# Kernel optimization log

Hardware: AMD Instinct MI355X
Metric: run time of the kernel (lower is better)

## Reference

```python
import jax, jax.numpy as jnp
import numpy as np

N_HEADS = 32
N_KV_HEADS = 8
HEAD_DIM = 64
DIM = 2048
MAX_CTX = 2048
N_REP = N_HEADS // N_KV_HEADS


def setup_inputs() -> dict:
    key = jax.random.key(0)
    ks = jax.random.split(key, 8)
    B, S = 1, 2048
    x = jax.random.normal(ks[0], (B, S, DIM), dtype=jnp.float32)
    # RoPE frequencies (real cos/sin, [S, head_dim//2])
    inv_freq = 1.0 / (10000.0 ** (np.arange(0, HEAD_DIM, 2, dtype=np.float32) / HEAD_DIM))
    t = np.arange(S, dtype=np.float32)
    freqs = np.outer(t, inv_freq)  # [S, HEAD_DIM//2]
    freqs_cos = jnp.asarray(np.cos(freqs), dtype=jnp.float32)
    freqs_sin = jnp.asarray(np.sin(freqs), dtype=jnp.float32)
    input_pos = jnp.arange(S, dtype=jnp.int32)
    scale = 0.02
    wq = jax.random.normal(ks[1], (N_HEADS * HEAD_DIM, DIM), dtype=jnp.float32) * scale
    wk = jax.random.normal(ks[2], (N_KV_HEADS * HEAD_DIM, DIM), dtype=jnp.float32) * scale
    wv = jax.random.normal(ks[3], (N_KV_HEADS * HEAD_DIM, DIM), dtype=jnp.float32) * scale
    wo = jax.random.normal(ks[4], (DIM, N_HEADS * HEAD_DIM), dtype=jnp.float32) * scale
    k_cache = jnp.zeros((B, N_KV_HEADS, MAX_CTX, HEAD_DIM), dtype=jnp.float32)
    v_cache = jnp.zeros((B, N_KV_HEADS, MAX_CTX, HEAD_DIM), dtype=jnp.float32)
    return {"x": x, "freqs_cos": freqs_cos, "freqs_sin": freqs_sin,
            "input_pos": input_pos, "wq": wq, "wk": wk, "wv": wv, "wo": wo,
            "k_cache": k_cache, "v_cache": v_cache}


def _apply_rope(x, cos, sin):
    # x: [B, S, H, HEAD_DIM]; cos/sin: [S, HEAD_DIM//2]
    xr = x[..., 0::2]
    xi = x[..., 1::2]
    c = cos[None, :, None, :]
    s = sin[None, :, None, :]
    out_r = xr * c - xi * s
    out_i = xr * s + xi * c
    # interleave back: stack on new trailing axis then flatten pairs
    out = jnp.stack([out_r, out_i], axis=-1)
    return out.reshape(x.shape)


def reference(x, freqs_cos, freqs_sin, input_pos, wq, wk, wv, wo, k_cache, v_cache):
    B, S, _ = x.shape
    q = (x @ wq.T).reshape(B, S, N_HEADS, HEAD_DIM)
    k = (x @ wk.T).reshape(B, S, N_KV_HEADS, HEAD_DIM)
    v = (x @ wv.T).reshape(B, S, N_KV_HEADS, HEAD_DIM)
    q = _apply_rope(q, freqs_cos, freqs_sin)
    k = _apply_rope(k, freqs_cos, freqs_sin)
    q = q.transpose(0, 2, 1, 3)   # [B, H, S, D]
    k = k.transpose(0, 2, 1, 3)   # [B, KV, S, D]
    v = v.transpose(0, 2, 1, 3)
    # KV-cache scatter update at input_pos
    k_full = k_cache.at[:, :, input_pos].set(k)   # [B, KV, MAX_CTX, D]
    v_full = v_cache.at[:, :, input_pos].set(v)
    # causal mask rows gathered at input_pos: [S, MAX_CTX]
    causal = jnp.tril(jnp.ones((MAX_CTX, MAX_CTX), dtype=bool))
    attn_mask = causal[input_pos]
    # GQA repeat_interleave along head dim
    k_rep = jnp.repeat(k_full, N_REP, axis=1)    # [B, H, MAX_CTX, D]
    v_rep = jnp.repeat(v_full, N_REP, axis=1)
    scale = 1.0 / jnp.sqrt(jnp.asarray(HEAD_DIM, dtype=x.dtype))
    scores = jnp.einsum('bhsd,bhtd->bhst', q, k_rep) * scale  # [B, H, S, MAX_CTX]
    neg = jnp.asarray(jnp.finfo(scores.dtype).min, dtype=scores.dtype)
    scores = jnp.where(attn_mask[None, None, :, :], scores, neg)
    attn = jax.nn.softmax(scores, axis=-1)
    y = jnp.einsum('bhst,bhtd->bhsd', attn, v_rep)  # [B, H, S, D]
    y = y.transpose(0, 2, 1, 3).reshape(B, S, N_HEADS * HEAD_DIM)
    return y @ wo.T
```

## Files before the change

### kernel.cpp

```cpp
#include <hip/hip_runtime.h>


typedef __attribute__((ext_vector_type(8))) __bf16 bf16x8;
typedef __attribute__((ext_vector_type(4))) float f32x4;

#define S_LEN 2048
#define DIMN  2048
#define NH    32
#define NKV   8
#define HD    64
#define QKVF  3072

__device__ __forceinline__ ushort f2bf(float f) {
  union { float f; unsigned u; } v; v.f = f;
  unsigned r = v.u + 0x7fffu + ((v.u >> 16) & 1u);
  return (ushort)(r >> 16);
}
__device__ __forceinline__ unsigned pack_bf2_rz(float a, float b) {
  union { float f; unsigned u; } va, vb; va.f = a; vb.f = b;
  return (va.u >> 16) | (vb.u & 0xffff0000u);
}
__device__ __forceinline__ float bf2f(ushort u) {
  union { unsigned u; float f; } v; v.u = ((unsigned)u) << 16;
  return v.f;
}
__device__ __forceinline__ void gld_lds16(const void* g, void* l) {
  __builtin_amdgcn_global_load_lds(
      (const __attribute__((address_space(1))) unsigned int*)g,
      (__attribute__((address_space(3))) unsigned int*)l, 16, 0, 0);
}

__global__ __launch_bounds__(256) void convert_all(
    const float* __restrict__ x, const float* __restrict__ wq,
    const float* __restrict__ wk, const float* __restrict__ wv,
    const float* __restrict__ wo, ushort* __restrict__ xb,
    ushort* __restrict__ wqkvb, ushort* __restrict__ wob) {
  const size_t NX = 4u * 1024 * 1024;
  const size_t NK = 1024 * 1024;
  size_t idx = ((size_t)blockIdx.x * 256 + threadIdx.x) * 4;
  const float* src; ushort* dst;
  if (idx < NX)                { src = x  + idx;                  dst = xb + idx; }
  else if (idx < 2 * NX)       { src = wq + (idx - NX);           dst = wqkvb + (idx - NX); }
  else if (idx < 2 * NX + NK)  { src = wk + (idx - 2 * NX);       dst = wqkvb + NX + (idx - 2 * NX); }
  else if (idx < 2 * NX + 2*NK){ src = wv + (idx - 2 * NX - NK);  dst = wqkvb + NX + NK + (idx - 2 * NX - NK); }
  else                         { src = wo + (idx - 2 * NX - 2*NK);dst = wob + (idx - 2 * NX - 2 * NK); }
  float4 v = *(const float4*)src;
  ushort4 o; o.x = f2bf(v.x); o.y = f2bf(v.y); o.z = f2bf(v.z); o.w = f2bf(v.w);
  *(ushort4*)dst = o;
}

template <int OUT_BF16, int BM, int BN>
__global__ __launch_bounds__(256) void gemm_bt(
    const ushort* __restrict__ A, const ushort* __restrict__ B,
    void* __restrict__ Cv, int M, int N, int K) {
  constexpr int IB = BM / 32;
  constexpr int JB = BN / 32;
  constexpr int NGA = BM / 8;
  constexpr int GPW = (BM + BN) / 32;
  __shared__ __align__(16) ushort As[2][BM * 64];
  __shared__ __align__(16) ushort Bs[2][BN * 64];
  const int n0 = blockIdx.x * BN, m0 = blockIdx.y * BM;
  const int t = threadIdx.x;
  const int lane = t & 63, wave = t >> 6;
  const int wm = (wave >> 1) * (BM / 2), wn = (wave & 1) * (BN / 2);
  const int col = lane & 15, quad = lane >> 4;
  const int sw = col & 7;
  const int lrow = lane >> 3;
  const int scol = ((lane & 7) ^ lrow) * 8;
  f32x4 acc[IB][JB] = {};

  auto stage = [&](int b, int kk) {
#pragma unroll
    for (int c = 0; c < GPW; ++c) {
      int g = wave * GPW + c;
      if (g < NGA)
        gld_lds16(&A[(size_t)(m0 + g * 8 + lrow) * K + kk + scol], &As[b][g * 8 * 64]);
      else
        gld_lds16(&B[(size_t)(n0 + (g - NGA) * 8 + lrow) * K + kk + scol],
                  &Bs[b][(g - NGA) * 8 * 64]);
    }
  };

  stage(0, 0);
  __syncthreads();
  for (int kk = 0; kk < K; kk += 64) {
    const int b = (kk >> 6) & 1;
    if (kk + 64 < K) stage(b ^ 1, kk + 64);
#pragma unroll
    for (int c = 0; c < 2; ++c) {
      const int chs = ((c * 4 + quad) ^ sw) * 8;
      bf16x8 af[IB], bfr[JB];
#pragma unroll
      for (int i = 0; i < IB; ++i)
        af[i] = *(const bf16x8*)&As[b][(wm + i * 16 + col) * 64 + chs];
#pragma unroll
      for (int j = 0; j < JB; ++j)
        bfr[j] = *(const bf16x8*)&Bs[b][(wn + j * 16 + col) * 64 + chs];
#pragma unroll
      for (int i = 0; i < IB; ++i)
#pragma unroll
        for (int j = 0; j < JB; ++j)
          acc[i][j] = __builtin_amdgcn_mfma_f32_16x16x32_bf16(af[i], bfr[j], acc[i][j], 0, 0, 0);
    }
    __syncthreads();
  }
#pragma unroll
  for (int i = 0; i < IB; ++i)
#pragma unroll
    for (int r = 0; r < 4; ++r) {
      int m = m0 + wm + i * 16 + quad * 4 + r;
      if (OUT_BF16) {
        ushort* C = (ushort*)Cv;
#pragma unroll
        for (int j = 0; j < JB; ++j)
          C[(size_t)m * N + n0 + wn + j * 16 + col] = f2bf(acc[i][j][r]);
      } else {
        float* C = (float*)Cv;
#pragma unroll
        for (int j = 0; j < JB; ++j)
          C[(size_t)m * N + n0 + wn + j * 16 + col] = acc[i][j][r];
      }
    }
}

__global__ __launch_bounds__(256) void rope_layout(
    const ushort* __restrict__ qkv, const float* __restrict__ fc,
    const float* __restrict__ fs, ushort* __restrict__ qb,
    ushort* __restrict__ kb, ushort* __restrict__ vt) {
  __shared__ ushort T[64][72];
  const int hh = blockIdx.x;
  const int s0 = blockIdx.y * 256;
  const int t = threadIdx.x;
  if (hh < 32) {
    ushort* dst = qb + (size_t)hh * S_LEN * 64;
    const float qs = 0.18033688011112042f;
    const int sr = t >> 4, dc = (t & 15) * 4, i0 = (t & 15) * 2;
#pragma unroll 4
    for (int pass = 0; pass < 16; ++pass) {
      int s = s0 + pass * 16 + sr;
      ushort4 vv = *(const ushort4*)&qkv[(size_t)s * QKVF + hh * 64 + dc];
      float2 cc = *(const float2*)&fc[s * 32 + i0];
      float2 ss = *(const float2*)&fs[s * 32 + i0];
      float xr0 = bf2f(vv.x), xi0 = bf2f(vv.y), xr1 = bf2f(vv.z), xi1 = bf2f(vv.w);
      ushort4 ov;
      ov.x = f2bf((xr0 * cc.x - xi0 * ss.x) * qs); ov.y = f2bf((xr0 * ss.x + xi0 * cc.x) * qs);
      ov.z = f2bf((xr1 * cc.y - xi1 * ss.y) * qs); ov.w = f2bf((xr1 * ss.y + xi1 * cc.y) * qs);
      *(ushort4*)&dst[(size_t)s * 64 + dc] = ov;
    }
  } else if (hh < 40) {
    const int kh2 = hh - 32;
    const int sr8 = t >> 3;
    const int ch = t & 7;
#pragma unroll 2
    for (int pass = 0; pass < 8; ++pass) {
      int s = s0 + pass * 32 + sr8;
      ushort in[8], out[8];
      *(int4*)&in[0] = *(const int4*)&qkv[(size_t)s * QKVF + 2048 + kh2 * 64 + ch * 8];
      float4 cc = *(const float4*)&fc[s * 32 + ch * 4];
      float4 ss4 = *(const float4*)&fs[s * 32 + ch * 4];
      const float* cp = &cc.x; const float* sp = &ss4.x;
#pragma unroll
      for (int i = 0; i < 4; ++i) {
        float xr = bf2f(in[2 * i]), xi = bf2f(in[2 * i + 1]);
        out[2 * i]     = f2bf(xr * cp[i] - xi * sp[i]);
        out[2 * i + 1] = f2bf(xr * sp[i] + xi * cp[i]);
      }
      int r = s & 63, tile = s >> 6;
      size_t pos = ((size_t)(kh2 * 32 + tile)) * 4096 +
                   ((size_t)(((ch >> 2) * 4 + (r >> 4)) * 64 + (ch & 3) * 16 + (r & 15))) * 8;
      *(int4*)&kb[pos] = *(const int4*)&out[0];
    }
  } else {
    const int vh = hh - 40;
    for (int sub = 0; sub < 4; ++sub) {
      int sb = s0 + sub * 64;
      int sr = t >> 2, dc = (t & 3) * 16;
      ushort tmp[16];
      *(int4*)&tmp[0] = *(const int4*)&qkv[(size_t)(sb + sr) * QKVF + 2560 + vh * 64 + dc];
      *(int4*)&tmp[8] = *(const int4*)&qkv[(size_t)(sb + sr) * QKVF + 2560 + vh * 64 + dc + 8];
      __syncthreads();
      const int pcol = ((sr & 15) << 2) | (sr >> 4);
#pragma unroll
      for (int k = 0; k < 16; ++k) T[dc + k][pcol] = tmp[k];
      __syncthreads();
      int d = t >> 2;
      int ch0 = (t & 3) * 2, ch1 = ch0 + 1;
      int tile = sb >> 6;
      size_t base = ((size_t)(vh * 32 + tile)) * 4096;
      size_t p0 = base + ((size_t)(((ch0 >> 2) * 4 + (d >> 4)) * 64 + (ch0 & 3) * 16 + (d & 15))) * 8;
      size_t p1 = base + ((size_t)(((ch1 >> 2) * 4 + (d >> 4)) * 64 + (ch1 & 3) * 16 + (d & 15))) * 8;
      *(int4*)&vt[p0] = *(const int4*)&T[d][ch0 * 8];
      *(int4*)&vt[p1] = *(const int4*)&T[d][ch1 * 8];
    }
  }
}

__global__ __launch_bounds__(256, 2) void attn(
    const ushort* __restrict__ qbg, const ushort* __restrict__ kbg,
    const ushort* __restrict__ vtg, ushort* __restrict__ yb) {
  __shared__ __align__(16) ushort Ps[4][2][16][64];
  const int kvh = blockIdx.x;
  const int y = blockIdx.y;
  const int sA = y, sB = 127 - y;
  const int ntA = (sA >> 2) + 1;
  const int ntB = (sB >> 2) + 1;
  const int wave = threadIdx.x >> 6;
  const int lane = threadIdx.x & 63;
  const int col = lane & 15, quad = lane >> 4;
  const int h = kvh * 4 + wave;
  const ushort* qh = qbg + (size_t)h * S_LEN * HD;
  const ushort* kbase = kbg + (size_t)kvh * 32 * 4096;
  const ushort* vbase = vtg + (size_t)kvh * 32 * 4096;

  const int q0A = sA * 16, q0B = sB * 16;
  bf16x8 qfA[2], qfB[2];
  qfA[0] = *(const bf16x8*)&qh[(size_t)(q0A + col) * HD + quad * 8];
  qfA[1] = *(const bf16x8*)&qh[(size_t)(q0A + col) * HD + 32 + quad * 8];
  qfB[0] = *(const bf16x8*)&qh[(size_t)(q0B + col) * HD + quad * 8];
  qfB[1] = *(const bf16x8*)&qh[(size_t)(q0B + col) * HD + 32 + quad * 8];
  float lA[4] = {}, lB[4] = {};
  f32x4 oA[4] = {}, oB[4] = {};

  bf16x8 k0[8], v0[8], k1[8], v1[8];

  auto loadK = [&](bf16x8 (&kf)[8], int t) {
    const ushort* kt = kbase + (size_t)t * 4096;
#pragma unroll
    for (int p = 0; p < 8; ++p) kf[p] = *(const bf16x8*)&kt[(p * 64 + lane) * 8];
  };
  auto loadV = [&](bf16x8 (&vf)[8], int t) {
    const ushort* vtt = vbase + (size_t)t * 4096;
#pragma unroll
    for (int p = 0; p < 8; ++p) vf[p] = *(const bf16x8*)&vtt[(p * 64 + lane) * 8];
  };

  auto body = [&](bf16x8 (&kfc)[8], bf16x8 (&vfc)[8],
                  bf16x8 (&kfn)[8], bf16x8 (&vfn)[8], int t) {
    const bool doA = (t < ntA);
    const bool maskA = (t == ntA - 1);
    const bool maskB = (t == ntB - 1);
    const bool pre = (t + 1 < ntB);
    if (pre) loadK(kfn, t + 1);
    f32x4 scA[4] = {}, scB[4] = {};
#pragma unroll
    for (int c = 0; c < 2; ++c)
#pragma unroll
      for (int j = 0; j < 4; ++j)
        scB[j] = __builtin_amdgcn_mfma_f32_16x16x32_bf16(qfB[c], kfc[c * 4 + j], scB[j], 0, 0, 0);
    if (doA) {
#pragma unroll
      for (int c = 0; c < 2; ++c)
#pragma unroll
        for (int j = 0; j < 4; ++j)
          scA[j] = __builtin_amdgcn_mfma_f32_16x16x32_bf16(qfA[c], kfc[c * 4 + j], scA[j], 0, 0, 0);
    }
#pragma unroll
    for (int r = 0; r < 4; ++r) {
      const int prow = quad * 4 + r;
      const int psw = (((col >> 1) ^ (prow & 7)) << 3) + ((col & 1) << 2);
      const int rowq = q0B + prow;
      float pr[4];
#pragma unroll
      for (int j = 0; j < 4; ++j) {
        float e = __builtin_amdgcn_exp2f(scB[j][r]);
        if (maskB) e = (t * 64 + j * 16 + col > rowq) ? 0.f : e;
        pr[j] = e;
      }
      lB[r] += (pr[0] + pr[1]) + (pr[2] + pr[3]);
      uint2 pk;
      pk.x = pack_bf2_rz(pr[0], pr[1]);
      pk.y = pack_bf2_rz(pr[2], pr[3]);
      *(uint2*)&Ps[wave][1][prow][psw] = pk;
    }
    if (doA) {
#pragma unroll
      for (int r = 0; r < 4; ++r) {
        const int prow = quad * 4 + r;
        const int psw = (((col >> 1) ^ (prow & 7)) << 3) + ((col & 1) << 2);
        const int rowq = q0A + prow;
        float pr[4];
#pragma unroll
        for (int j = 0; j < 4; ++j) {
          float e = __builtin_amdgcn_exp2f(scA[j][r]);
          if (maskA) e = (t * 64 + j * 16 + col > rowq) ? 0.f : e;
          pr[j] = e;
        }
        lA[r] += (pr[0] + pr[1]) + (pr[2] + pr[3]);
        uint2 pk;
        pk.x = pack_bf2_rz(pr[0], pr[1]);
        pk.y = pack_bf2_rz(pr[2], pr[3]);
        *(uint2*)&Ps[wave][0][prow][psw] = pk;
      }
    }
    if (pre) loadV(vfn, t + 1);
#pragma unroll
    for (int c = 0; c < 2; ++c) {
      const int psr = ((c * 4 + quad) ^ (col & 7)) * 8;
      bf16x8 pfB = *(const bf16x8*)&Ps[wave][1][col][psr];
#pragma unroll
      for (int db = 0; db < 4; ++db)
        oB[db] = __builtin_amdgcn_mfma_f32_16x16x32_bf16(pfB, vfc[c * 4 + db], oB[db], 0, 0, 0);
    }
    if (doA) {
#pragma unroll
      for (int c = 0; c < 2; ++c) {
        const int psr = ((c * 4 + quad) ^ (col & 7)) * 8;
        bf16x8 pfA = *(const bf16x8*)&Ps[wave][0][col][psr];
#pragma unroll
        for (int db = 0; db < 4; ++db)
          oA[db] = __builtin_amdgcn_mfma_f32_16x16x32_bf16(pfA, vfc[c * 4 + db], oA[db], 0, 0, 0);
      }
    }
  };

  loadK(k0, 0);
  loadV(v0, 0);
  for (int t = 0; t < ntB;) {
    body(k0, v0, k1, v1, t);
    ++t;
    if (t >= ntB) break;
    body(k1, v1, k0, v0, t);
    ++t;
  }

  auto write_out = [&](const f32x4 (&o)[4], const float (&l)[4], int q0) {
#pragma unroll
    for (int r = 0; r < 4; ++r) {
      float ls = l[r];
      ls += __shfl_xor(ls, 1);
      ls += __shfl_xor(ls, 2);
      ls += __shfl_xor(ls, 4);
      ls += __shfl_xor(ls, 8);
      float inv = 1.0f / ls;
      int rowq = q0 + quad * 4 + r;
#pragma unroll
      for (int db = 0; db < 4; ++db)
        yb[(size_t)rowq * (NH * HD) + h * HD + db * 16 + col] = f2bf(o[db][r] * inv);
    }
  };
  write_out(oA, lA, q0A);
  write_out(oB, lB, q0B);
}

extern "C" void kernel_launch(void* const* d_in, const int* in_sizes, int n_in,
                              void* d_out, int out_size, void* d_ws, size_t ws_size,
                              hipStream_t stream) {
  (void)in_sizes; (void)n_in; (void)out_size; (void)ws_size;
  const float* x  = (const float*)d_in[0];
  const float* fc = (const float*)d_in[1];
  const float* fs = (const float*)d_in[2];
  const float* wq = (const float*)d_in[4];
  const float* wk = (const float*)d_in[5];
  const float* wv = (const float*)d_in[6];
  const float* wo = (const float*)d_in[7];
  ushort* w = (ushort*)d_ws;
  const size_t M1 = 1024 * 1024;
  ushort* xb    = w;
  ushort* wqkvb = w + 4 * M1;
  ushort* wob   = w + 10 * M1;
  ushort* qkvb  = w + 14 * M1;
  ushort* qb    = w + 20 * M1;
  ushort* kb    = w + 24 * M1;
  ushort* vt    = w + 25 * M1;
  ushort* yb    = w + 26 * M1;

  convert_all<<<14336, 256, 0, stream>>>(x, wq, wk, wv, wo, xb, wqkvb, wob);
  gemm_bt<1, 128, 96><<<dim3(QKVF / 96, S_LEN / 128), 256, 0, stream>>>(xb, wqkvb, qkvb, S_LEN, QKVF, DIMN);
  rope_layout<<<dim3(48, 8), 256, 0, stream>>>(qkvb, fc, fs, qb, kb, vt);
  attn<<<dim3(NKV, 64), 256, 0, stream>>>(qb, kb, vt, yb);
  gemm_bt<0, 64, 128><<<dim3(DIMN / 128, S_LEN / 64), 256, 0, stream>>>(yb, wob, d_out, S_LEN, DIMN, NH * HD);
}
```

Before: 213.1 us.

## Split attention KV tiles across two blocks and merge partials in a new kernel

Attention now launches a third grid dimension. Each z-slice handles alternating KV tiles (even or odd) and prefetches two tiles ahead. Each slice writes unnormalised fp32 partial outputs and row sums, and a new merge_norm kernel adds the two halves, normalises and writes bf16. The aim is to double the number of attention blocks and raise occupancy (launch bounds 2 to 4) so the GPU is better filled. The cost is extra fp32 partial-buffer traffic, one more kernel launch, and possible register spills under the tighter occupancy bound. The merge only works because the kernel uses no running max, so partials can simply be summed.

```diff
diff --git a/kernel.cpp b/kernel.cpp
--- a/kernel.cpp
+++ b/kernel.cpp
@@ -195,12 +195,14 @@
   }
 }
 
-__global__ __launch_bounds__(256, 2) void attn(
+__global__ __launch_bounds__(256, 4) void attn(
     const ushort* __restrict__ qbg, const ushort* __restrict__ kbg,
-    const ushort* __restrict__ vtg, ushort* __restrict__ yb) {
+    const ushort* __restrict__ vtg, float* __restrict__ obuf,
+    float* __restrict__ lbuf) {
   __shared__ __align__(16) ushort Ps[4][2][16][64];
   const int kvh = blockIdx.x;
   const int y = blockIdx.y;
+  const int khalf = blockIdx.z;
   const int sA = y, sB = 127 - y;
   const int ntA = (sA >> 2) + 1;
   const int ntB = (sB >> 2) + 1;
@@ -211,6 +213,8 @@
   const ushort* qh = qbg + (size_t)h * S_LEN * HD;
   const ushort* kbase = kbg + (size_t)kvh * 32 * 4096;
   const ushort* vbase = vtg + (size_t)kvh * 32 * 4096;
+  float* obase = obuf + ((size_t)(khalf * 32 + h)) * S_LEN * HD;
+  float* lbase = lbuf + ((size_t)(khalf * 32 + h)) * S_LEN;
 
   const int q0A = sA * 16, q0B = sB * 16;
   bf16x8 qfA[2], qfB[2];
@@ -239,8 +243,8 @@
     const bool doA = (t < ntA);
     const bool maskA = (t == ntA - 1);
     const bool maskB = (t == ntB - 1);
-    const bool pre = (t + 1 < ntB);
-    if (pre) loadK(kfn, t + 1);
+    const bool pre = (t + 2 < ntB);
+    if (pre) loadK(kfn, t + 2);
     f32x4 scA[4] = {}, scB[4] = {};
 #pragma unroll
     for (int c = 0; c < 2; ++c)
@@ -292,7 +296,7 @@
         *(uint2*)&Ps[wave][0][prow][psw] = pk;
       }
     }
-    if (pre) loadV(vfn, t + 1);
+    if (pre) loadV(vfn, t + 2);
 #pragma unroll
     for (int c = 0; c < 2; ++c) {
       const int psr = ((c * 4 + quad) ^ (col & 7)) * 8;
@@ -313,33 +317,60 @@
     }
   };
 
-  loadK(k0, 0);
-  loadV(v0, 0);
-  for (int t = 0; t < ntB;) {
-    body(k0, v0, k1, v1, t);
-    ++t;
-    if (t >= ntB) break;
-    body(k1, v1, k0, v0, t);
-    ++t;
+  {
+    int t = khalf;
+    loadK(k0, t);
+    loadV(v0, t);
+    for (;;) {
+      body(k0, v0, k1, v1, t);
+      t += 2;
+      if (t >= ntB) break;
+      body(k1, v1, k0, v0, t);
+      t += 2;
+      if (t >= ntB) break;
+    }
   }
 
-  auto write_out = [&](const f32x4 (&o)[4], const float (&l)[4], int q0) {
+  auto write_part = [&](const f32x4 (&o)[4], const float (&l)[4], int q0) {
 #pragma unroll
     for (int r = 0; r < 4; ++r) {
+      const int rowq = q0 + quad * 4 + r;
+#pragma unroll
+      for (int db = 0; db < 4; ++db)
+        obase[(size_t)rowq * HD + db * 16 + col] = o[db][r];
       float ls = l[r];
       ls += __shfl_xor(ls, 1);
       ls += __shfl_xor(ls, 2);
       ls += __shfl_xor(ls, 4);
       ls += __shfl_xor(ls, 8);
-      float inv = 1.0f / ls;
-      int rowq = q0 + quad * 4 + r;
-#pragma unroll
-      for (int db = 0; db < 4; ++db)
-        yb[(size_t)rowq * (NH * HD) + h * HD + db * 16 + col] = f2bf(o[db][r] * inv);
+      if (col == 0) lbase[rowq] = ls;
     }
   };
-  write_out(oA, lA, q0A);
-  write_out(oB, lB, q0B);
+  write_part(oA, lA, q0A);
+  write_part(oB, lB, q0B);
+}
+
+__global__ __launch_bounds__(256) void merge_norm(
+    const float* __restrict__ obuf, const float* __restrict__ lbuf,
+    ushort* __restrict__ yb) {
+  const size_t OKH = (size_t)32 * S_LEN * HD;
+  const size_t LKH = (size_t)32 * S_LEN;
+  int idx = blockIdx.x * 256 + threadIdx.x;
+  int dg = idx & 15;
+  int row = (idx >> 4) & (S_LEN - 1);
+  int h = idx >> 15;
+  const float* o0 = obuf + ((size_t)h * S_LEN + row) * HD + dg * 4;
+  const float* o1 = o0 + OKH;
+  float4 a = *(const float4*)o0;
+  float4 b = *(const float4*)o1;
+  float l = lbuf[(size_t)h * S_LEN + row] + lbuf[LKH + (size_t)h * S_LEN + row];
+  float inv = 1.0f / l;
+  ushort4 o;
+  o.x = f2bf((a.x + b.x) * inv);
+  o.y = f2bf((a.y + b.y) * inv);
+  o.z = f2bf((a.z + b.z) * inv);
+  o.w = f2bf((a.w + b.w) * inv);
+  *(ushort4*)&yb[(size_t)row * (NH * HD) + h * HD + dg * 4] = o;
 }
 
 extern "C" void kernel_launch(void* const* d_in, const int* in_sizes, int n_in,
@@ -363,10 +394,13 @@
   ushort* kb    = w + 24 * M1;
   ushort* vt    = w + 25 * M1;
   ushort* yb    = w + 26 * M1;
+  float*  obuf  = (float*)(w + 30 * M1);
+  float*  lbuf  = obuf + (size_t)2 * 32 * S_LEN * HD;
 
   convert_all<<<14336, 256, 0, stream>>>(x, wq, wk, wv, wo, xb, wqkvb, wob);
   gemm_bt<1, 128, 96><<<dim3(QKVF / 96, S_LEN / 128), 256, 0, stream>>>(xb, wqkvb, qkvb, S_LEN, QKVF, DIMN);
   rope_layout<<<dim3(48, 8), 256, 0, stream>>>(qkvb, fc, fs, qb, kb, vt);
-  attn<<<dim3(NKV, 64), 256, 0, stream>>>(qb, kb, vt, yb);
+  attn<<<dim3(NKV, 64, 2), 256, 0, stream>>>(qb, kb, vt, obuf, lbuf);
+  merge_norm<<<4096, 256, 0, stream>>>(obuf, lbuf, yb);
   gemm_bt<0, 64, 128><<<dim3(DIMN / 128, S_LEN / 64), 256, 0, stream>>>(yb, wob, d_out, S_LEN, DIMN, NH * HD);
 }
```

After: 494.6 us. +132.1%, slower.
